# Kernel tuning notes

Hardware: AMD Instinct MI355X
Metric: run time of the kernel (lower is better)

Reference implementation:

```python
import jax, jax.numpy as jnp
import numpy as np

B, S, D, K = 128, 200, 128, 4
NQ, NC = 10000, 500


def setup_inputs() -> dict:
    key = jax.random.key(0)
    ks = jax.random.split(key, 20)
    f = jnp.float32
    inp = {}
    inp["question_seq"] = jax.random.randint(ks[0], (B, S), 0, NQ)
    inp["hint_attempt_seq"] = jax.random.randint(ks[1], (B, S), 0, 12)
    inp["correct_seq"] = jax.random.randint(ks[2], (B, S), 0, 2)
    inp["interval_time_seq"] = jax.random.randint(ks[3], (B, S), 0, 100)
    inp["use_time_seq"] = jax.random.randint(ks[4], (B, S), 0, 100)
    inp["q2c_table"] = jax.random.randint(ks[5], (NQ, K), 0, NC)
    inp["q2c_mask_table"] = jax.random.randint(ks[6], (NQ, K), 0, 2)
    s = 0.1
    inp["embed_question"] = jax.random.normal(ks[7], (NQ, D), f) * s
    inp["embed_question_disc"] = jax.random.normal(ks[8], (NQ, 1), f) * s
    inp["embed_concept"] = jax.random.normal(ks[9], (NC, D), f) * s
    inp["embed_interval_time"] = jax.random.normal(ks[10], (100, D), f) * s
    inp["embed_use_time"] = jax.random.normal(ks[11], (100, D), f) * s
    inp["embed_hint_attempt"] = jax.random.normal(ks[12], (12, D), f) * s
    inp["W_fuse"] = jax.random.normal(ks[13], (2 * D, D), f) / np.float32(np.sqrt(2 * D))
    inp["b_fuse"] = jnp.zeros((D,), f)
    inp["W_absorb"] = jax.random.normal(ks[14], (3 * D, D), f) / np.float32(np.sqrt(3 * D))
    inp["b_absorb"] = jnp.zeros((D,), f)
    inp["W_forget"] = jax.random.normal(ks[15], (3 * D, D), f) / np.float32(np.sqrt(3 * D))
    inp["b_forget"] = jnp.zeros((D,), f)
    inp["latent0"] = jax.random.normal(ks[16], (B, D), f) * 0.1  # xavier-init latent_pre
    return inp


def _cos(a, b, eps=1e-8):
    # torch.cosine_similarity semantics with eps clamp on each norm
    num = jnp.sum(a * b, axis=-1)
    na = jnp.sqrt(jnp.sum(a * a, axis=-1))
    nb = jnp.sqrt(jnp.sum(b * b, axis=-1))
    return num / (jnp.maximum(na, eps) * jnp.maximum(nb, eps))


def _forward(question_seq, hint_attempt_seq, correct_seq, interval_time_seq, use_time_seq,
             q2c_table, q2c_mask_table,
             embed_question, embed_question_disc, embed_concept, embed_interval_time,
             embed_use_time, embed_hint_attempt,
             W_fuse, b_fuse, W_absorb, b_absorb, W_forget, b_forget, latent0):
    f = latent0.dtype
    qe = embed_question[question_seq]                                # [B,S,D]
    qd = jax.nn.sigmoid(embed_question_disc[question_seq]) * 10.0    # [B,S,1]
    ce = jnp.broadcast_to(correct_seq.astype(f)[:, :, None], qe.shape)  # [B,S,D]
    ite = embed_interval_time[interval_time_seq]                     # [B,S,D]
    ute = embed_use_time[use_time_seq]                               # [B,S,D]
    hae = embed_hint_attempt[hint_attempt_seq]                       # [B,S,D]
    cp = embed_concept[q2c_table[question_seq]]                      # [B,S,K,D]
    m = q2c_mask_table[question_seq].astype(f)                       # [B,S,K]

    tm = lambda x: jnp.swapaxes(x, 0, 1)  # time-major for scan
    xs = (tm(qe[:, :-1]), tm(ce[:, :-1]), tm(ute[:, :-1]), tm(hae[:, :-1]), tm(ite[:, :-1]),
          tm(cp[:, :-1]), tm(cp[:, 1:]), tm(qd[:, 1:]), tm(m[:, :-1]))

    def step(lp, x):
        qe_t, ce_t, ute_t, hae_t, ite_t, cp_t, cp_t1, qd_t1, m_t = x
        inter = jnp.concatenate([qe_t, ce_t], axis=-1) @ W_fuse + b_fuse
        absorb = jnp.concatenate([inter, ute_t, hae_t], axis=-1) @ W_absorb + b_absorb
        forget = jax.nn.sigmoid(jnp.concatenate([lp, ite_t, inter], axis=-1) @ W_forget + b_forget)
        lc = lp * forget + absorb  # dropout p=0 -> identity
        qdiff = (_cos(qe_t[:, None, :], cp_t) + 1.0) * 0.5   # [B,K]
        uab = (_cos(lc[:, None, :], cp_t1) + 1.0) * 0.5      # [B,K]
        logit = qd_t1[:, 0] * jnp.sum((uab - qdiff) * m_t, axis=-1)  # [B]
        return lc, jax.nn.sigmoid(logit)

    _, ys = jax.lax.scan(step, latent0, xs)  # ys: [S-1, B]
    y = jnp.concatenate([ys.T, jnp.zeros((latent0.shape[0], 1), f)], axis=1)  # [B,S], last col 0
    return y


def reference(question_seq, hint_attempt_seq, correct_seq, interval_time_seq, use_time_seq,
              q2c_table, q2c_mask_table,
              embed_question, embed_question_disc, embed_concept, embed_interval_time,
              embed_use_time, embed_hint_attempt,
              W_fuse, b_fuse, W_absorb, b_absorb, W_forget, b_forget, latent0):
    return _forward(question_seq, hint_attempt_seq, correct_seq, interval_time_seq, use_time_seq,
                    q2c_table, q2c_mask_table,
                    embed_question, embed_question_disc, embed_concept, embed_interval_time,
                    embed_use_time, embed_hint_attempt,
                    W_fuse, b_fuse, W_absorb, b_absorb, W_forget, b_forget, latent0)
```

## Files before the change

### kernel.cpp

```cpp
#include <hip/hip_runtime.h>
#include <hip/hip_bf16.h>

typedef unsigned short u16;

#define Bb  128
#define Ss  200
#define Tt  199
#define Dd  128
#define Kk  4
#define NQq 10000
#define NCc 500
#define CHK 16
#define NCH 13

__device__ inline float bf2f(u16 u) {
    union { unsigned int i; float f; } x;
    x.i = ((unsigned int)u) << 16;
    return x.f;
}

__device__ inline float ldf(const void* p, int i, int m) {
    if (m) return ((const float*)p)[i];
    return bf2f(((const u16*)p)[i]);
}

__device__ inline void stf(void* p, int i, int m, float v) {
    if (m) ((float*)p)[i] = v;
    else ((__hip_bfloat16*)p)[i] = __float2bfloat16(v);
}

__device__ inline int clampi(int v, int lo, int hi) {
    return v < lo ? lo : (v > hi ? hi : v);
}

__device__ inline float wave_red(float v) {
#pragma unroll
    for (int m = 32; m >= 1; m >>= 1) v += __shfl_xor(v, m);
    return v;
}

__device__ inline float4 f4add(float4 a, float4 b) {
    return make_float4(a.x + b.x, a.y + b.y, a.z + b.z, a.w + b.w);
}
__device__ inline float4 f4fma(float s, float4 a, float4 b) {
    return make_float4(fmaf(s, a.x, b.x), fmaf(s, a.y, b.y),
                       fmaf(s, a.z, b.z), fmaf(s, a.w, b.w));
}

__device__ inline int detect_mode(const void* Eq) {
    const u16* q = (const u16*)Eq;
    const int l = threadIdx.x & 63;
    float mx = 0.f;
#pragma unroll
    for (int k = 0; k < 4; ++k) {
        float a = fabsf(bf2f(q[l * 4 + k]));
        if (!(a == a)) a = 3.0e38f;
        mx = fmaxf(mx, a);
    }
#pragma unroll
    for (int s = 32; s >= 1; s >>= 1) mx = fmaxf(mx, __shfl_xor(mx, s));
    return (mx > 1.0e6f) ? 1 : 0;
}

__global__ __launch_bounds__(128) void k_prep(
    const void* Eq, const void* Wf, const void* Wa, const void* Wg,
    const void* bfu, const void* ba, const void* bg,
    const void* Eut, const void* Eha, const void* Eit, const void* Ec,
    float* cnorm, float* BabT, float* BfgT,
    float* vA0, float* vA1, float* vF0, float* vF1,
    float* PA_ut, float* PA_ha, float* PF_it) {
    const int m = detect_mode(Eq);
    const int bi = blockIdx.x, tid = threadIdx.x;
    __shared__ float cs2s[128];
    __shared__ float tmp[2];
    if (bi < 500) {
        const int c = bi;
        float v = ldf(Ec, c * 128 + tid, m);
        float s = wave_red(v * v);
        if ((tid & 63) == 0) tmp[tid >> 6] = s;
        __syncthreads();
        if (tid == 0) cnorm[c] = fmaxf(sqrtf(tmp[0] + tmp[1]), 1e-8f);
    } else if (bi < 628) {
        const int r = bi - 500;
        float acc = 0.f;
        for (int j = 0; j < 128; ++j)
            acc += ldf(Wf, r * 128 + j, m) * ldf(Wa, j * 128 + tid, m);
        BabT[r * 128 + tid] = acc;
    } else if (bi < 756) {
        const int r = bi - 628;
        float acc = 0.f;
        for (int j = 0; j < 128; ++j)
            acc += ldf(Wf, r * 128 + j, m) * ldf(Wg, (256 + j) * 128 + tid, m);
        BfgT[r * 128 + tid] = acc;
    } else if (bi == 756) {
        float s = 0.f;
        for (int r = 0; r < 128; ++r) s += ldf(Wf, (128 + r) * 128 + tid, m);
        cs2s[tid] = s;
        __syncthreads();
        float a0 = 0.f, a1 = 0.f;
        for (int j = 0; j < 128; ++j) {
            float wv = ldf(Wa, j * 128 + tid, m);
            a0 += ldf(bfu, j, m) * wv;
            a1 += cs2s[j] * wv;
        }
        vA0[tid] = a0 + ldf(ba, tid, m);
        vA1[tid] = a1;
    } else if (bi == 757) {
        float s = 0.f;
        for (int r = 0; r < 128; ++r) s += ldf(Wf, (128 + r) * 128 + tid, m);
        cs2s[tid] = s;
        __syncthreads();
        float a0 = 0.f, a1 = 0.f;
        for (int j = 0; j < 128; ++j) {
            float wv = ldf(Wg, (256 + j) * 128 + tid, m);
            a0 += ldf(bfu, j, m) * wv;
            a1 += cs2s[j] * wv;
        }
        vF0[tid] = a0 + ldf(bg, tid, m);
        vF1[tid] = a1;
    } else if (bi < 858) {
        const int r = bi - 758;
        float acc = 0.f;
        for (int j = 0; j < 128; ++j)
            acc += ldf(Eut, r * 128 + j, m) * ldf(Wa, (128 + j) * 128 + tid, m);
        PA_ut[r * 128 + tid] = acc;
    } else if (bi < 870) {
        const int r = bi - 858;
        float acc = 0.f;
        for (int j = 0; j < 128; ++j)
            acc += ldf(Eha, r * 128 + j, m) * ldf(Wa, (256 + j) * 128 + tid, m);
        PA_ha[r * 128 + tid] = acc;
    } else {
        const int r = bi - 870;
        float acc = 0.f;
        for (int j = 0; j < 128; ++j)
            acc += ldf(Eit, r * 128 + j, m) * ldf(Wg, (128 + j) * 128 + tid, m);
        PF_it[r * 128 + tid] = acc;
    }
}

__global__ __launch_bounds__(256) void k_mid(
    const void* Eq, const void* Eqd, const void* Ec,
    const int* q2c, const int* q2cm,
    const float* BabT, const float* BfgT, const float* cnorm,
    float* PA_q, float* PF_q, float* qdm, float* qd10) {
    const int m = detect_mode(Eq);
    const int tid = threadIdx.x;
    const int bi = blockIdx.x;
    if (bi < 313) {
        __shared__ float At[32][36];
        __shared__ float Bt0[32][128];
        __shared__ float Bt1[32][128];
        const int r0 = bi * 32;
        float acc0[2][8], acc1[2][8];
#pragma unroll
        for (int j = 0; j < 2; ++j)
#pragma unroll
            for (int i = 0; i < 8; ++i) { acc0[j][i] = 0.f; acc1[j][i] = 0.f; }
        const int tx = tid & 15, ty = tid >> 4;
        for (int ks = 0; ks < 4; ++ks) {
            {
                const int row = tid >> 3, seg = tid & 7;
                const int q = clampi(r0 + row, 0, NQq - 1);
                const int ei = q * 128 + ks * 32 + seg * 4;
                float* dst = &At[row][seg * 4];
                if (m) {
                    float4 v = *(const float4*)((const float*)Eq + ei);
                    dst[0] = v.x; dst[1] = v.y; dst[2] = v.z; dst[3] = v.w;
                } else {
                    uint2 v = *(const uint2*)((const u16*)Eq + ei);
                    dst[0] = bf2f((u16)(v.x & 0xffff)); dst[1] = bf2f((u16)(v.x >> 16));
                    dst[2] = bf2f((u16)(v.y & 0xffff)); dst[3] = bf2f((u16)(v.y >> 16));
                }
            }
            {
                const float4* s0 = (const float4*)(BabT + ks * 32 * 128);
                const float4* s1 = (const float4*)(BfgT + ks * 32 * 128);
                float4* d0 = (float4*)&Bt0[0][0];
                float4* d1 = (float4*)&Bt1[0][0];
#pragma unroll
                for (int k = 0; k < 4; ++k) {
                    d0[tid + k * 256] = s0[tid + k * 256];
                    d1[tid + k * 256] = s1[tid + k * 256];
                }
            }
            __syncthreads();
#pragma unroll
            for (int kk = 0; kk < 32; kk += 4) {
                float a_[2][4];
                *(float4*)&a_[0][0] = *(const float4*)&At[ty * 2 + 0][kk];
                *(float4*)&a_[1][0] = *(const float4*)&At[ty * 2 + 1][kk];
#pragma unroll
                for (int q = 0; q < 4; ++q) {
                    float4 b0 = *(const float4*)&Bt0[kk + q][tx * 8];
                    float4 b1 = *(const float4*)&Bt0[kk + q][tx * 8 + 4];
                    float4 c0 = *(const float4*)&Bt1[kk + q][tx * 8];
                    float4 c1 = *(const float4*)&Bt1[kk + q][tx * 8 + 4];
#pragma unroll
                    for (int j = 0; j < 2; ++j) {
                        const float av = a_[j][q];
                        acc0[j][0] += av * b0.x; acc0[j][1] += av * b0.y;
                        acc0[j][2] += av * b0.z; acc0[j][3] += av * b0.w;
                        acc0[j][4] += av * b1.x; acc0[j][5] += av * b1.y;
                        acc0[j][6] += av * b1.z; acc0[j][7] += av * b1.w;
                        acc1[j][0] += av * c0.x; acc1[j][1] += av * c0.y;
                        acc1[j][2] += av * c0.z; acc1[j][3] += av * c0.w;
                        acc1[j][4] += av * c1.x; acc1[j][5] += av * c1.y;
                        acc1[j][6] += av * c1.z; acc1[j][7] += av * c1.w;
                    }
                }
            }
            __syncthreads();
        }
#pragma unroll
        for (int j = 0; j < 2; ++j) {
            const int q = r0 + ty * 2 + j;
            if (q < NQq) {
                float* oa = PA_q + q * 128 + tx * 8;
                float* of = PF_q + q * 128 + tx * 8;
#pragma unroll
                for (int i = 0; i < 8; ++i) { oa[i] = acc0[j][i]; of[i] = acc1[j][i]; }
            }
        }
    } else {
        const int wv = tid >> 6, lane = tid & 63;
        const int q = (bi - 313) * 4 + wv;
        const float qa = ldf(Eq, q * 128 + lane, m);
        const float qb = ldf(Eq, q * 128 + 64 + lane, m);
        const float nqc = fmaxf(sqrtf(wave_red(qa * qa + qb * qb)), 1e-8f);
        const int4 cc = ((const int4*)q2c)[q];
        const int4 mm = ((const int4*)q2cm)[q];
        const int cks[4] = {clampi(cc.x, 0, NCc - 1), clampi(cc.y, 0, NCc - 1),
                            clampi(cc.z, 0, NCc - 1), clampi(cc.w, 0, NCc - 1)};
        const int ms[4]  = {mm.x, mm.y, mm.z, mm.w};
        float qs = 0.f;
#pragma unroll
        for (int k = 0; k < 4; ++k) {
            const int ck = cks[k];
            float dot = wave_red(qa * ldf(Ec, ck * 128 + lane, m) +
                                 qb * ldf(Ec, ck * 128 + 64 + lane, m));
            qs += (float)ms[k] * (0.5f * dot / (nqc * cnorm[ck]) + 0.5f);
        }
        if (lane == 0) {
            qdm[q] = qs;
            qd10[q] = 10.f / (1.f + __expf(-ldf(Eqd, q, m)));
        }
    }
}

__global__ __launch_bounds__(256) void p4_scan(
    const int* q_seq, const int* ut_seq, const int* ha_seq, const int* it_seq,
    const int* c_seq,
    const void* Eq, const void* Wg, const void* L0,
    const float* PA_q, const float* PA_ut, const float* PA_ha,
    const float* PF_q, const float* PF_it,
    const float* vA0, const float* vA1, const float* vF0, const float* vF1,
    float* lc_seq) {
    const int m = detect_mode(Eq);
    const int b = blockIdx.x;
    const int tid = threadIdx.x;
    const int wv = tid >> 6, l = tid & 63;
    const int d0 = 2 * l;
    const int ib = wv << 5;
    const int dd = ib + (l & 31);

    __shared__ float part[2][4][128];
    __shared__ float st_ab[CHK * 128];
    __shared__ float st_pf[CHK * 128];

    float wA[32], wB[32];
#pragma unroll
    for (int k = 0; k < 32; ++k) {
        wA[k] = ldf(Wg, (ib + k) * 128 + d0, m);
        wB[k] = ldf(Wg, (ib + k) * 128 + d0 + 1, m);
    }
    float lc = (l < 32) ? ldf(L0, b * 128 + dd, m) : 0.f;

    const int srow = tid >> 4, seg = tid & 15;
    const int off8 = seg * 8;
    const float4 A0a = *(const float4*)(vA0 + off8), A0b = *(const float4*)(vA0 + off8 + 4);
    const float4 A1a = *(const float4*)(vA1 + off8), A1b = *(const float4*)(vA1 + off8 + 4);
    const float4 F0a = *(const float4*)(vF0 + off8), F0b = *(const float4*)(vF0 + off8 + 4);
    const float4 F1a = *(const float4*)(vF1 + off8), F1b = *(const float4*)(vF1 + off8 + 4);

    float4 qa0, qa1, ua0, ua1, ga0, ga1, qf0, qf1, if0, if1;
    float cf;
#define LOAD_CHUNK(C)                                                          \
    {                                                                          \
        int tt = (C) * CHK + srow; if (tt > Tt - 1) tt = Tt - 1;               \
        const int base = b * Ss + tt;                                          \
        const int qt = clampi(q_seq[base], 0, NQq - 1);                        \
        const int ut = clampi(ut_seq[base], 0, 99);                            \
        const int ha = clampi(ha_seq[base], 0, 11);                            \
        const int it = clampi(it_seq[base], 0, 99);                            \
        cf = (float)c_seq[base];                                               \
        const float* pq = PA_q + qt * 128 + off8;                              \
        qa0 = *(const float4*)pq; qa1 = *(const float4*)(pq + 4);              \
        const float* pu = PA_ut + ut * 128 + off8;                             \
        ua0 = *(const float4*)pu; ua1 = *(const float4*)(pu + 4);              \
        const float* ph = PA_ha + ha * 128 + off8;                             \
        ga0 = *(const float4*)ph; ga1 = *(const float4*)(ph + 4);              \
        const float* pf = PF_q + qt * 128 + off8;                              \
        qf0 = *(const float4*)pf; qf1 = *(const float4*)(pf + 4);              \
        const float* pi = PF_it + it * 128 + off8;                             \
        if0 = *(const float4*)pi; if1 = *(const float4*)(pi + 4);              \
    }

    LOAD_CHUNK(0)
    float lcbuf[CHK];
    int par = 0;

    for (int c = 0; c < NCH; ++c) {
        __syncthreads();
        {
            float4 ab0 = f4fma(cf, A1a, f4add(f4add(qa0, ua0), f4add(ga0, A0a)));
            float4 ab1 = f4fma(cf, A1b, f4add(f4add(qa1, ua1), f4add(ga1, A0b)));
            float4 pf0 = f4fma(cf, F1a, f4add(qf0, f4add(if0, F0a)));
            float4 pf1 = f4fma(cf, F1b, f4add(qf1, f4add(if1, F0b)));
            float4* sa = (float4*)(st_ab + srow * 128 + off8);
            sa[0] = ab0; sa[1] = ab1;
            float4* sp = (float4*)(st_pf + srow * 128 + off8);
            sp[0] = pf0; sp[1] = pf1;
        }
        if (c + 1 < NCH) LOAD_CHUNK(c + 1)
        __syncthreads();

#pragma unroll
        for (int s = 0; s < CHK; ++s) {
            float pa = 0.f, pb = 0.f;
#pragma unroll
            for (int k = 0; k < 32; ++k) {
                const float u = __uint_as_float(
                    __builtin_amdgcn_readlane(__float_as_uint(lc), k));
                pa = fmaf(u, wA[k], pa);
                pb = fmaf(u, wB[k], pb);
            }
            *(float2*)&part[par][wv][d0] = make_float2(pa, pb);
            __syncthreads();
            if (l < 32) {
                const float fs = part[par][0][dd] + part[par][1][dd]
                               + part[par][2][dd] + part[par][3][dd];
                const float ab = st_ab[(s << 7) + dd];
                const float pf = st_pf[(s << 7) + dd];
                const float fg = 1.f / (1.f + __expf(-(fs + pf)));
                lc = lc * fg + ab;
                lcbuf[s] = lc;
            }
            par ^= 1;
        }
        if (l < 32) {
#pragma unroll
            for (int s = 0; s < CHK; ++s) {
                const int t = c * CHK + s;
                if (t < Tt)
                    lc_seq[((long)t * 128 + b) * 128 + dd] = lcbuf[s];
            }
        }
    }
#undef LOAD_CHUNK
}

__global__ __launch_bounds__(256) void p5_out(
    const int* q_seq, const int* q2c, const int* q2cm,
    const float* lc_seq, const float* qdm, const float* qd10,
    const float* cnorm, const void* Eq, const void* Ec, void* out) {
    const int m = detect_mode(Eq);
    const int wv = threadIdx.x >> 6, lane = threadIdx.x & 63;
    const int r = blockIdx.x * 4 + wv;
    const int t = r >> 7, b = r & 127;
    const int qt  = clampi(q_seq[b * Ss + t], 0, NQq - 1);
    const int qt1 = clampi(q_seq[b * Ss + t + 1], 0, NQq - 1);
    const int4 mm = ((const int4*)q2cm)[qt];
    int4 ci = ((const int4*)q2c)[qt1];
    const int c0 = clampi(ci.x, 0, NCc - 1), c1 = clampi(ci.y, 0, NCc - 1);
    const int c2 = clampi(ci.z, 0, NCc - 1), c3 = clampi(ci.w, 0, NCc - 1);
    const float la = lc_seq[(long)r * 128 + lane];
    const float lb = lc_seq[(long)r * 128 + 64 + lane];
    float nl = la * la + lb * lb;
    float d0 = la * ldf(Ec, c0 * 128 + lane, m) + lb * ldf(Ec, c0 * 128 + 64 + lane, m);
    float d1 = la * ldf(Ec, c1 * 128 + lane, m) + lb * ldf(Ec, c1 * 128 + 64 + lane, m);
    float d2 = la * ldf(Ec, c2 * 128 + lane, m) + lb * ldf(Ec, c2 * 128 + 64 + lane, m);
    float d3 = la * ldf(Ec, c3 * 128 + lane, m) + lb * ldf(Ec, c3 * 128 + 64 + lane, m);
#pragma unroll
    for (int s = 32; s >= 1; s >>= 1) {
        nl += __shfl_xor(nl, s);
        d0 += __shfl_xor(d0, s); d1 += __shfl_xor(d1, s);
        d2 += __shfl_xor(d2, s); d3 += __shfl_xor(d3, s);
    }
    if (lane == 0) {
        const float inl = 1.f / fmaxf(sqrtf(nl), 1e-8f);
        const float accv = (float)mm.x * (0.5f * d0 * inl / cnorm[c0] + 0.5f)
                         + (float)mm.y * (0.5f * d1 * inl / cnorm[c1] + 0.5f)
                         + (float)mm.z * (0.5f * d2 * inl / cnorm[c2] + 0.5f)
                         + (float)mm.w * (0.5f * d3 * inl / cnorm[c3] + 0.5f);
        const float logit = qd10[qt1] * (accv - qdm[qt]);
        stf(out, b * Ss + t, m, 1.f / (1.f + __expf(-logit)));
        if (t == 0) stf(out, b * Ss + 199, m, 0.f);
    }
}

extern "C" void kernel_launch(void* const* d_in, const int* in_sizes, int n_in,
                              void* d_out, int out_size, void* d_ws, size_t ws_size,
                              hipStream_t stream) {
    (void)in_sizes; (void)n_in; (void)out_size; (void)ws_size;
    const int* q_seq  = (const int*)d_in[0];
    const int* ha_seq = (const int*)d_in[1];
    const int* c_seq  = (const int*)d_in[2];
    const int* it_seq = (const int*)d_in[3];
    const int* ut_seq = (const int*)d_in[4];
    const int* q2c    = (const int*)d_in[5];
    const int* q2cm   = (const int*)d_in[6];
    const void* Eq   = d_in[7];
    const void* Eqd  = d_in[8];
    const void* Ec   = d_in[9];
    const void* Eit  = d_in[10];
    const void* Eut  = d_in[11];
    const void* Eha  = d_in[12];
    const void* Wf   = d_in[13];
    const void* bfu  = d_in[14];
    const void* Wa   = d_in[15];
    const void* ba   = d_in[16];
    const void* Wg   = d_in[17];
    const void* bg   = d_in[18];
    const void* L0   = d_in[19];

    float* cnorm = (float*)d_ws;
    float* vA0   = cnorm + 512;
    float* vA1   = vA0 + 128;
    float* vF0   = vA1 + 128;
    float* vF1   = vF0 + 128;
    float* BabT  = vF1 + 128;
    float* BfgT  = BabT + 16384;
    float* PA_ut = BfgT + 16384;
    float* PA_ha = PA_ut + 12800;
    float* PF_it = PA_ha + 1536;
    float* qdm   = PF_it + 12800;
    float* qd10  = qdm + 10016;
    float* PA_q  = qd10 + 10016;
    float* PF_q  = PA_q + 1280000;
    float* lc_seq= PF_q + 1280000;

    hipLaunchKernelGGL(k_prep, dim3(970), dim3(128), 0, stream,
                       Eq, Wf, Wa, Wg, bfu, ba, bg, Eut, Eha, Eit, Ec,
                       cnorm, BabT, BfgT, vA0, vA1, vF0, vF1, PA_ut, PA_ha, PF_it);
    hipLaunchKernelGGL(k_mid, dim3(2813), dim3(256), 0, stream,
                       Eq, Eqd, Ec, q2c, q2cm, BabT, BfgT, cnorm,
                       PA_q, PF_q, qdm, qd10);
    hipLaunchKernelGGL(p4_scan, dim3(Bb), dim3(256), 0, stream,
                       q_seq, ut_seq, ha_seq, it_seq, c_seq, Eq, Wg, L0,
                       PA_q, PA_ut, PA_ha, PF_q, PF_it,
                       vA0, vA1, vF0, vF1, lc_seq);
    hipLaunchKernelGGL(p5_out, dim3(Tt * Bb / 4), dim3(256), 0, stream,
                       q_seq, q2c, q2cm, lc_seq, qdm, qd10, cnorm, Eq, Ec, d_out);
}
```

Measured before the change: 235.4 us.

## Fuse all four stages into one persistent cooperative kernel with grid syncs

Replaces the four separate launches (prep, mid, scan, output) with one cooperative kernel of 512 blocks that loops over job indices and separates the phases with grid-wide syncs. Concept norms are now recomputed inline instead of stored in a cnorm table, and the prep jobs pair two outputs per 256-thread block. This targets launch overhead and idle gaps between small dependent kernels. In exchange, work is throttled to the persistent grid size, and the serial scan phase runs on only 128 blocks while the rest wait at the final barrier.

```diff
diff --git a/kernel.cpp b/kernel.cpp
--- a/kernel.cpp
+++ b/kernel.cpp
@@ -1,17 +1,19 @@
 #include <hip/hip_runtime.h>
 #include <hip/hip_bf16.h>
+#include <hip/hip_cooperative_groups.h>
+
+namespace cg = cooperative_groups;
 
 typedef unsigned short u16;
 
 #define Bb  128
 #define Ss  200
 #define Tt  199
-#define Dd  128
-#define Kk  4
 #define NQq 10000
 #define NCc 500
 #define CHK 16
 #define NCH 13
+#define GRID 512
 
 __device__ inline float bf2f(u16 u) {
     union { unsigned int i; float f; } x;
@@ -62,340 +64,339 @@
     return (mx > 1.0e6f) ? 1 : 0;
 }
 
-__global__ __launch_bounds__(128) void k_prep(
-    const void* Eq, const void* Wf, const void* Wa, const void* Wg,
-    const void* bfu, const void* ba, const void* bg,
-    const void* Eut, const void* Eha, const void* Eit, const void* Ec,
-    float* cnorm, float* BabT, float* BfgT,
-    float* vA0, float* vA1, float* vF0, float* vF1,
-    float* PA_ut, float* PA_ha, float* PF_it) {
-    const int m = detect_mode(Eq);
-    const int bi = blockIdx.x, tid = threadIdx.x;
-    __shared__ float cs2s[128];
-    __shared__ float tmp[2];
-    if (bi < 500) {
-        const int c = bi;
-        float v = ldf(Ec, c * 128 + tid, m);
-        float s = wave_red(v * v);
-        if ((tid & 63) == 0) tmp[tid >> 6] = s;
-        __syncthreads();
-        if (tid == 0) cnorm[c] = fmaxf(sqrtf(tmp[0] + tmp[1]), 1e-8f);
-    } else if (bi < 628) {
-        const int r = bi - 500;
-        float acc = 0.f;
-        for (int j = 0; j < 128; ++j)
-            acc += ldf(Wf, r * 128 + j, m) * ldf(Wa, j * 128 + tid, m);
-        BabT[r * 128 + tid] = acc;
-    } else if (bi < 756) {
-        const int r = bi - 628;
-        float acc = 0.f;
-        for (int j = 0; j < 128; ++j)
-            acc += ldf(Wf, r * 128 + j, m) * ldf(Wg, (256 + j) * 128 + tid, m);
-        BfgT[r * 128 + tid] = acc;
-    } else if (bi == 756) {
-        float s = 0.f;
-        for (int r = 0; r < 128; ++r) s += ldf(Wf, (128 + r) * 128 + tid, m);
-        cs2s[tid] = s;
-        __syncthreads();
-        float a0 = 0.f, a1 = 0.f;
-        for (int j = 0; j < 128; ++j) {
-            float wv = ldf(Wa, j * 128 + tid, m);
-            a0 += ldf(bfu, j, m) * wv;
-            a1 += cs2s[j] * wv;
-        }
-        vA0[tid] = a0 + ldf(ba, tid, m);
-        vA1[tid] = a1;
-    } else if (bi == 757) {
-        float s = 0.f;
-        for (int r = 0; r < 128; ++r) s += ldf(Wf, (128 + r) * 128 + tid, m);
-        cs2s[tid] = s;
-        __syncthreads();
-        float a0 = 0.f, a1 = 0.f;
-        for (int j = 0; j < 128; ++j) {
-            float wv = ldf(Wg, (256 + j) * 128 + tid, m);
-            a0 += ldf(bfu, j, m) * wv;
-            a1 += cs2s[j] * wv;
-        }
-        vF0[tid] = a0 + ldf(bg, tid, m);
-        vF1[tid] = a1;
-    } else if (bi < 858) {
-        const int r = bi - 758;
-        float acc = 0.f;
-        for (int j = 0; j < 128; ++j)
-            acc += ldf(Eut, r * 128 + j, m) * ldf(Wa, (128 + j) * 128 + tid, m);
-        PA_ut[r * 128 + tid] = acc;
-    } else if (bi < 870) {
-        const int r = bi - 858;
-        float acc = 0.f;
-        for (int j = 0; j < 128; ++j)
-            acc += ldf(Eha, r * 128 + j, m) * ldf(Wa, (256 + j) * 128 + tid, m);
-        PA_ha[r * 128 + tid] = acc;
-    } else {
-        const int r = bi - 870;
-        float acc = 0.f;
-        for (int j = 0; j < 128; ++j)
-            acc += ldf(Eit, r * 128 + j, m) * ldf(Wg, (128 + j) * 128 + tid, m);
-        PF_it[r * 128 + tid] = acc;
+struct KArgs {
+    const int *q_seq, *ha_seq, *c_seq, *it_seq, *ut_seq, *q2c, *q2cm;
+    const void *Eq, *Eqd, *Ec, *Eit, *Eut, *Eha;
+    const void *Wf, *bfu, *Wa, *ba, *Wg, *bg, *L0;
+    float *BabT, *BfgT, *vA0, *vA1, *vF0, *vF1;
+    float *PA_ut, *PA_ha, *PF_it, *qdm, *qd10, *PA_q, *PF_q, *lc_seq;
+    void* out;
+};
+
+__global__ __launch_bounds__(256, 4) void k_fused(KArgs a) {
+    cg::grid_group grid = cg::this_grid();
+    __shared__ __align__(16) float smemf[9344];
+    const int m = detect_mode(a.Eq);
+    const int tid = threadIdx.x;
+    const int nb = gridDim.x;
+
+    for (int job = blockIdx.x; job < 241; job += nb) {
+        if (job < 128) {
+            const int r = job, col = tid & 127;
+            float acc = 0.f;
+            if (tid < 128) {
+                for (int j = 0; j < 128; ++j)
+                    acc += ldf(a.Wf, r * 128 + j, m) * ldf(a.Wa, j * 128 + col, m);
+                a.BabT[r * 128 + col] = acc;
+            } else {
+                for (int j = 0; j < 128; ++j)
+                    acc += ldf(a.Wf, r * 128 + j, m) * ldf(a.Wg, (256 + j) * 128 + col, m);
+                a.BfgT[r * 128 + col] = acc;
+            }
+        } else if (job == 128) {
+            const int col = tid & 127;
+            if (tid < 128) {
+                float s = 0.f;
+                for (int r2 = 0; r2 < 128; ++r2) s += ldf(a.Wf, (128 + r2) * 128 + col, m);
+                smemf[col] = s;
+            }
+            __syncthreads();
+            float a0 = 0.f, a1 = 0.f;
+            if (tid < 128) {
+                for (int j = 0; j < 128; ++j) {
+                    const float wv = ldf(a.Wa, j * 128 + col, m);
+                    a0 += ldf(a.bfu, j, m) * wv;
+                    a1 += smemf[j] * wv;
+                }
+                a.vA0[col] = a0 + ldf(a.ba, col, m);
+                a.vA1[col] = a1;
+            } else {
+                for (int j = 0; j < 128; ++j) {
+                    const float wv = ldf(a.Wg, (256 + j) * 128 + col, m);
+                    a0 += ldf(a.bfu, j, m) * wv;
+                    a1 += smemf[j] * wv;
+                }
+                a.vF0[col] = a0 + ldf(a.bg, col, m);
+                a.vF1[col] = a1;
+            }
+            __syncthreads();
+        } else if (job < 229) {
+            const int r = job - 129, col = tid & 127;
+            float acc = 0.f;
+            if (tid < 128) {
+                for (int j = 0; j < 128; ++j)
+                    acc += ldf(a.Eut, r * 128 + j, m) * ldf(a.Wa, (128 + j) * 128 + col, m);
+                a.PA_ut[r * 128 + col] = acc;
+            } else {
+                for (int j = 0; j < 128; ++j)
+                    acc += ldf(a.Eit, r * 128 + j, m) * ldf(a.Wg, (128 + j) * 128 + col, m);
+                a.PF_it[r * 128 + col] = acc;
+            }
+        } else {
+            const int r = job - 229;
+            if (tid < 128) {
+                float acc = 0.f;
+                for (int j = 0; j < 128; ++j)
+                    acc += ldf(a.Eha, r * 128 + j, m) * ldf(a.Wa, (256 + j) * 128 + tid, m);
+                a.PA_ha[r * 128 + tid] = acc;
+            }
+        }
     }
-}
-
-__global__ __launch_bounds__(256) void k_mid(
-    const void* Eq, const void* Eqd, const void* Ec,
-    const int* q2c, const int* q2cm,
-    const float* BabT, const float* BfgT, const float* cnorm,
-    float* PA_q, float* PF_q, float* qdm, float* qd10) {
-    const int m = detect_mode(Eq);
-    const int tid = threadIdx.x;
-    const int bi = blockIdx.x;
-    if (bi < 313) {
-        __shared__ float At[32][36];
-        __shared__ float Bt0[32][128];
-        __shared__ float Bt1[32][128];
-        const int r0 = bi * 32;
-        float acc0[2][8], acc1[2][8];
-#pragma unroll
-        for (int j = 0; j < 2; ++j)
-#pragma unroll
-            for (int i = 0; i < 8; ++i) { acc0[j][i] = 0.f; acc1[j][i] = 0.f; }
-        const int tx = tid & 15, ty = tid >> 4;
-        for (int ks = 0; ks < 4; ++ks) {
+    __threadfence();
+    grid.sync();
+
+    {
+        float* At  = smemf;
+        float* Bt0 = smemf + 1152;
+        float* Bt1 = smemf + 5248;
+        for (int job = blockIdx.x; job < 2813; job += nb) {
+            if (job < 313) {
+                const int r0 = job * 32;
+                float acc0[2][8], acc1[2][8];
+#pragma unroll
+                for (int j = 0; j < 2; ++j)
+#pragma unroll
+                    for (int i = 0; i < 8; ++i) { acc0[j][i] = 0.f; acc1[j][i] = 0.f; }
+                const int tx = tid & 15, ty = tid >> 4;
+                for (int ks = 0; ks < 4; ++ks) {
+                    {
+                        const int row = tid >> 3, seg = tid & 7;
+                        const int q = clampi(r0 + row, 0, NQq - 1);
+                        const int ei = q * 128 + ks * 32 + seg * 4;
+                        float* dst = At + row * 36 + seg * 4;
+                        if (m) {
+                            float4 v = *(const float4*)((const float*)a.Eq + ei);
+                            dst[0] = v.x; dst[1] = v.y; dst[2] = v.z; dst[3] = v.w;
+                        } else {
+                            uint2 v = *(const uint2*)((const u16*)a.Eq + ei);
+                            dst[0] = bf2f((u16)(v.x & 0xffff)); dst[1] = bf2f((u16)(v.x >> 16));
+                            dst[2] = bf2f((u16)(v.y & 0xffff)); dst[3] = bf2f((u16)(v.y >> 16));
+                        }
+                    }
+                    {
+                        const float4* s0 = (const float4*)(a.BabT + ks * 32 * 128);
+                        const float4* s1 = (const float4*)(a.BfgT + ks * 32 * 128);
+                        float4* d0 = (float4*)Bt0;
+                        float4* d1 = (float4*)Bt1;
+#pragma unroll
+                        for (int k = 0; k < 4; ++k) {
+                            d0[tid + k * 256] = s0[tid + k * 256];
+                            d1[tid + k * 256] = s1[tid + k * 256];
+                        }
+                    }
+                    __syncthreads();
+#pragma unroll
+                    for (int kk = 0; kk < 32; kk += 4) {
+                        float a_[2][4];
+                        *(float4*)&a_[0][0] = *(const float4*)(At + (ty * 2 + 0) * 36 + kk);
+                        *(float4*)&a_[1][0] = *(const float4*)(At + (ty * 2 + 1) * 36 + kk);
+#pragma unroll
+                        for (int q = 0; q < 4; ++q) {
+                            float4 b0 = *(const float4*)(Bt0 + (kk + q) * 128 + tx * 8);
+                            float4 b1 = *(const float4*)(Bt0 + (kk + q) * 128 + tx * 8 + 4);
+                            float4 c0 = *(const float4*)(Bt1 + (kk + q) * 128 + tx * 8);
+                            float4 c1 = *(const float4*)(Bt1 + (kk + q) * 128 + tx * 8 + 4);
+#pragma unroll
+                            for (int j = 0; j < 2; ++j) {
+                                const float av = a_[j][q];
+                                acc0[j][0] += av * b0.x; acc0[j][1] += av * b0.y;
+                                acc0[j][2] += av * b0.z; acc0[j][3] += av * b0.w;
+                                acc0[j][4] += av * b1.x; acc0[j][5] += av * b1.y;
+                                acc0[j][6] += av * b1.z; acc0[j][7] += av * b1.w;
+                                acc1[j][0] += av * c0.x; acc1[j][1] += av * c0.y;
+                                acc1[j][2] += av * c0.z; acc1[j][3] += av * c0.w;
+                                acc1[j][4] += av * c1.x; acc1[j][5] += av * c1.y;
+                                acc1[j][6] += av * c1.z; acc1[j][7] += av * c1.w;
+                            }
+                        }
+                    }
+                    __syncthreads();
+                }
+#pragma unroll
+                for (int j = 0; j < 2; ++j) {
+                    const int q = r0 + ty * 2 + j;
+                    if (q < NQq) {
+                        float* oa = a.PA_q + q * 128 + tx * 8;
+                        float* of = a.PF_q + q * 128 + tx * 8;
+#pragma unroll
+                        for (int i = 0; i < 8; ++i) { oa[i] = acc0[j][i]; of[i] = acc1[j][i]; }
+                    }
+                }
+            } else {
+                const int wv = tid >> 6, lane = tid & 63;
+                const int q = (job - 313) * 4 + wv;
+                const float qa = ldf(a.Eq, q * 128 + lane, m);
+                const float qb = ldf(a.Eq, q * 128 + 64 + lane, m);
+                const float nqc = fmaxf(sqrtf(wave_red(qa * qa + qb * qb)), 1e-8f);
+                const int4 cc = ((const int4*)a.q2c)[q];
+                const int4 mm = ((const int4*)a.q2cm)[q];
+                const int cks[4] = {clampi(cc.x, 0, NCc - 1), clampi(cc.y, 0, NCc - 1),
+                                    clampi(cc.z, 0, NCc - 1), clampi(cc.w, 0, NCc - 1)};
+                const int ms[4]  = {mm.x, mm.y, mm.z, mm.w};
+                float qs = 0.f;
+#pragma unroll
+                for (int k = 0; k < 4; ++k) {
+                    const int ck = cks[k];
+                    const float ea = ldf(a.Ec, ck * 128 + lane, m);
+                    const float eb = ldf(a.Ec, ck * 128 + 64 + lane, m);
+                    const float dot = wave_red(qa * ea + qb * eb);
+                    const float nn = fmaxf(sqrtf(wave_red(ea * ea + eb * eb)), 1e-8f);
+                    qs += (float)ms[k] * (0.5f * dot / (nqc * nn) + 0.5f);
+                }
+                if (lane == 0) {
+                    a.qdm[q] = qs;
+                    a.qd10[q] = 10.f / (1.f + __expf(-ldf(a.Eqd, q, m)));
+                }
+            }
+        }
+    }
+    __threadfence();
+    grid.sync();
+
+    if (blockIdx.x < 128) {
+        float* part  = smemf;
+        float* st_ab = smemf + 1024;
+        float* st_pf = smemf + 3072;
+        const int b = blockIdx.x;
+        const int wv = tid >> 6, l = tid & 63;
+        const int d0 = 2 * l;
+        const int ib = wv << 5;
+        const int dd = ib + (l & 31);
+
+        float wA[32], wB[32];
+#pragma unroll
+        for (int k = 0; k < 32; ++k) {
+            wA[k] = ldf(a.Wg, (ib + k) * 128 + d0, m);
+            wB[k] = ldf(a.Wg, (ib + k) * 128 + d0 + 1, m);
+        }
+        float lc = (l < 32) ? ldf(a.L0, b * 128 + dd, m) : 0.f;
+
+        const int srow = tid >> 4, seg = tid & 15;
+        const int off8 = seg * 8;
+        const float4 A0a = *(const float4*)(a.vA0 + off8), A0b = *(const float4*)(a.vA0 + off8 + 4);
+        const float4 A1a = *(const float4*)(a.vA1 + off8), A1b = *(const float4*)(a.vA1 + off8 + 4);
+        const float4 F0a = *(const float4*)(a.vF0 + off8), F0b = *(const float4*)(a.vF0 + off8 + 4);
+        const float4 F1a = *(const float4*)(a.vF1 + off8), F1b = *(const float4*)(a.vF1 + off8 + 4);
+
+        float4 qa0, qa1, ua0, ua1, ga0, ga1, qf0, qf1, if0, if1;
+        float cf;
+#define LOAD_CHUNK(C)                                                          \
+        {                                                                      \
+            int tt = (C) * CHK + srow; if (tt > Tt - 1) tt = Tt - 1;           \
+            const int base = b * Ss + tt;                                      \
+            const int qt = clampi(a.q_seq[base], 0, NQq - 1);                  \
+            const int ut = clampi(a.ut_seq[base], 0, 99);                      \
+            const int ha = clampi(a.ha_seq[base], 0, 11);                      \
+            const int it = clampi(a.it_seq[base], 0, 99);                      \
+            cf = (float)a.c_seq[base];                                         \
+            const float* pq = a.PA_q + qt * 128 + off8;                        \
+            qa0 = *(const float4*)pq; qa1 = *(const float4*)(pq + 4);          \
+            const float* pu = a.PA_ut + ut * 128 + off8;                       \
+            ua0 = *(const float4*)pu; ua1 = *(const float4*)(pu + 4);          \
+            const float* ph = a.PA_ha + ha * 128 + off8;                       \
+            ga0 = *(const float4*)ph; ga1 = *(const float4*)(ph + 4);          \
+            const float* pf = a.PF_q + qt * 128 + off8;                        \
+            qf0 = *(const float4*)pf; qf1 = *(const float4*)(pf + 4);          \
+            const float* pi = a.PF_it + it * 128 + off8;                       \
+            if0 = *(const float4*)pi; if1 = *(const float4*)(pi + 4);          \
+        }
+
+        LOAD_CHUNK(0)
+        float lcbuf[CHK];
+        int par = 0;
+
+        for (int c = 0; c < NCH; ++c) {
+            __syncthreads();
             {
-                const int row = tid >> 3, seg = tid & 7;
-                const int q = clampi(r0 + row, 0, NQq - 1);
-                const int ei = q * 128 + ks * 32 + seg * 4;
-                float* dst = &At[row][seg * 4];
-                if (m) {
-                    float4 v = *(const float4*)((const float*)Eq + ei);
-                    dst[0] = v.x; dst[1] = v.y; dst[2] = v.z; dst[3] = v.w;
-                } else {
-                    uint2 v = *(const uint2*)((const u16*)Eq + ei);
-                    dst[0] = bf2f((u16)(v.x & 0xffff)); dst[1] = bf2f((u16)(v.x >> 16));
-                    dst[2] = bf2f((u16)(v.y & 0xffff)); dst[3] = bf2f((u16)(v.y >> 16));
-                }
-            }
-            {
-                const float4* s0 = (const float4*)(BabT + ks * 32 * 128);
-                const float4* s1 = (const float4*)(BfgT + ks * 32 * 128);
-                float4* d0 = (float4*)&Bt0[0][0];
-                float4* d1 = (float4*)&Bt1[0][0];
-#pragma unroll
-                for (int k = 0; k < 4; ++k) {
-                    d0[tid + k * 256] = s0[tid + k * 256];
-                    d1[tid + k * 256] = s1[tid + k * 256];
-                }
-            }
+                float4 ab0 = f4fma(cf, A1a, f4add(f4add(qa0, ua0), f4add(ga0, A0a)));
+                float4 ab1 = f4fma(cf, A1b, f4add(f4add(qa1, ua1), f4add(ga1, A0b)));
+                float4 pf0 = f4fma(cf, F1a, f4add(qf0, f4add(if0, F0a)));
+                float4 pf1 = f4fma(cf, F1b, f4add(qf1, f4add(if1, F0b)));
+                float4* sa = (float4*)(st_ab + srow * 128 + off8);
+                sa[0] = ab0; sa[1] = ab1;
+                float4* sp = (float4*)(st_pf + srow * 128 + off8);
+                sp[0] = pf0; sp[1] = pf1;
+            }
+            if (c + 1 < NCH) LOAD_CHUNK(c + 1)
             __syncthreads();
-#pragma unroll
-            for (int kk = 0; kk < 32; kk += 4) {
-                float a_[2][4];
-                *(float4*)&a_[0][0] = *(const float4*)&At[ty * 2 + 0][kk];
-                *(float4*)&a_[1][0] = *(const float4*)&At[ty * 2 + 1][kk];
-#pragma unroll
-                for (int q = 0; q < 4; ++q) {
-                    float4 b0 = *(const float4*)&Bt0[kk + q][tx * 8];
-                    float4 b1 = *(const float4*)&Bt0[kk + q][tx * 8 + 4];
-                    float4 c0 = *(const float4*)&Bt1[kk + q][tx * 8];
-                    float4 c1 = *(const float4*)&Bt1[kk + q][tx * 8 + 4];
-#pragma unroll
-                    for (int j = 0; j < 2; ++j) {
-                        const float av = a_[j][q];
-                        acc0[j][0] += av * b0.x; acc0[j][1] += av * b0.y;
-                        acc0[j][2] += av * b0.z; acc0[j][3] += av * b0.w;
-                        acc0[j][4] += av * b1.x; acc0[j][5] += av * b1.y;
-                        acc0[j][6] += av * b1.z; acc0[j][7] += av * b1.w;
-                        acc1[j][0] += av * c0.x; acc1[j][1] += av * c0.y;
-                        acc1[j][2] += av * c0.z; acc1[j][3] += av * c0.w;
-                        acc1[j][4] += av * c1.x; acc1[j][5] += av * c1.y;
-                        acc1[j][6] += av * c1.z; acc1[j][7] += av * c1.w;
-                    }
-                }
-            }
-            __syncthreads();
-        }
-#pragma unroll
-        for (int j = 0; j < 2; ++j) {
-            const int q = r0 + ty * 2 + j;
-            if (q < NQq) {
-                float* oa = PA_q + q * 128 + tx * 8;
-                float* of = PF_q + q * 128 + tx * 8;
-#pragma unroll
-                for (int i = 0; i < 8; ++i) { oa[i] = acc0[j][i]; of[i] = acc1[j][i]; }
-            }
-        }
-    } else {
+
+#pragma unroll
+            for (int s = 0; s < CHK; ++s) {
+                float pa = 0.f, pb = 0.f;
+#pragma unroll
+                for (int k = 0; k < 32; ++k) {
+                    const float u = __uint_as_float(
+                        __builtin_amdgcn_readlane(__float_as_uint(lc), k));
+                    pa = fmaf(u, wA[k], pa);
+                    pb = fmaf(u, wB[k], pb);
+                }
+                *(float2*)(part + par * 512 + wv * 128 + d0) = make_float2(pa, pb);
+                __syncthreads();
+                if (l < 32) {
+                    const float fs = part[par * 512 + 0 * 128 + dd] + part[par * 512 + 1 * 128 + dd]
+                                   + part[par * 512 + 2 * 128 + dd] + part[par * 512 + 3 * 128 + dd];
+                    const float ab = st_ab[(s << 7) + dd];
+                    const float pf = st_pf[(s << 7) + dd];
+                    const float fg = 1.f / (1.f + __expf(-(fs + pf)));
+                    lc = lc * fg + ab;
+                    lcbuf[s] = lc;
+                }
+                par ^= 1;
+            }
+            if (l < 32) {
+#pragma unroll
+                for (int s = 0; s < CHK; ++s) {
+                    const int t = c * CHK + s;
+                    if (t < Tt)
+                        a.lc_seq[((long)t * 128 + b) * 128 + dd] = lcbuf[s];
+                }
+            }
+        }
+#undef LOAD_CHUNK
+    }
+    __threadfence();
+    grid.sync();
+
+    for (int job = blockIdx.x; job < 6368; job += nb) {
         const int wv = tid >> 6, lane = tid & 63;
-        const int q = (bi - 313) * 4 + wv;
-        const float qa = ldf(Eq, q * 128 + lane, m);
-        const float qb = ldf(Eq, q * 128 + 64 + lane, m);
-        const float nqc = fmaxf(sqrtf(wave_red(qa * qa + qb * qb)), 1e-8f);
-        const int4 cc = ((const int4*)q2c)[q];
-        const int4 mm = ((const int4*)q2cm)[q];
-        const int cks[4] = {clampi(cc.x, 0, NCc - 1), clampi(cc.y, 0, NCc - 1),
-                            clampi(cc.z, 0, NCc - 1), clampi(cc.w, 0, NCc - 1)};
-        const int ms[4]  = {mm.x, mm.y, mm.z, mm.w};
-        float qs = 0.f;
-#pragma unroll
-        for (int k = 0; k < 4; ++k) {
-            const int ck = cks[k];
-            float dot = wave_red(qa * ldf(Ec, ck * 128 + lane, m) +
-                                 qb * ldf(Ec, ck * 128 + 64 + lane, m));
-            qs += (float)ms[k] * (0.5f * dot / (nqc * cnorm[ck]) + 0.5f);
+        const int r = job * 4 + wv;
+        const int t = r >> 7, b = r & 127;
+        const int qt  = clampi(a.q_seq[b * Ss + t], 0, NQq - 1);
+        const int qt1 = clampi(a.q_seq[b * Ss + t + 1], 0, NQq - 1);
+        const int4 mm = ((const int4*)a.q2cm)[qt];
+        int4 ci = ((const int4*)a.q2c)[qt1];
+        const int c0 = clampi(ci.x, 0, NCc - 1), c1 = clampi(ci.y, 0, NCc - 1);
+        const int c2 = clampi(ci.z, 0, NCc - 1), c3 = clampi(ci.w, 0, NCc - 1);
+        const float la = a.lc_seq[(long)r * 128 + lane];
+        const float lb = a.lc_seq[(long)r * 128 + 64 + lane];
+        const float e0a = ldf(a.Ec, c0 * 128 + lane, m), e0b = ldf(a.Ec, c0 * 128 + 64 + lane, m);
+        const float e1a = ldf(a.Ec, c1 * 128 + lane, m), e1b = ldf(a.Ec, c1 * 128 + 64 + lane, m);
+        const float e2a = ldf(a.Ec, c2 * 128 + lane, m), e2b = ldf(a.Ec, c2 * 128 + 64 + lane, m);
+        const float e3a = ldf(a.Ec, c3 * 128 + lane, m), e3b = ldf(a.Ec, c3 * 128 + 64 + lane, m);
+        float nl = la * la + lb * lb;
+        float d0 = la * e0a + lb * e0b, n0 = e0a * e0a + e0b * e0b;
+        float d1 = la * e1a + lb * e1b, n1 = e1a * e1a + e1b * e1b;
+        float d2 = la * e2a + lb * e2b, n2 = e2a * e2a + e2b * e2b;
+        float d3 = la * e3a + lb * e3b, n3 = e3a * e3a + e3b * e3b;
+#pragma unroll
+        for (int s = 32; s >= 1; s >>= 1) {
+            nl += __shfl_xor(nl, s);
+            d0 += __shfl_xor(d0, s); d1 += __shfl_xor(d1, s);
+            d2 += __shfl_xor(d2, s); d3 += __shfl_xor(d3, s);
+            n0 += __shfl_xor(n0, s); n1 += __shfl_xor(n1, s);
+            n2 += __shfl_xor(n2, s); n3 += __shfl_xor(n3, s);
         }
         if (lane == 0) {
-            qdm[q] = qs;
-            qd10[q] = 10.f / (1.f + __expf(-ldf(Eqd, q, m)));
-        }
-    }
-}
-
-__global__ __launch_bounds__(256) void p4_scan(
-    const int* q_seq, const int* ut_seq, const int* ha_seq, const int* it_seq,
-    const int* c_seq,
-    const void* Eq, const void* Wg, const void* L0,
-    const float* PA_q, const float* PA_ut, const float* PA_ha,
-    const float* PF_q, const float* PF_it,
-    const float* vA0, const float* vA1, const float* vF0, const float* vF1,
-    float* lc_seq) {
-    const int m = detect_mode(Eq);
-    const int b = blockIdx.x;
-    const int tid = threadIdx.x;
-    const int wv = tid >> 6, l = tid & 63;
-    const int d0 = 2 * l;
-    const int ib = wv << 5;
-    const int dd = ib + (l & 31);
-
-    __shared__ float part[2][4][128];
-    __shared__ float st_ab[CHK * 128];
-    __shared__ float st_pf[CHK * 128];
-
-    float wA[32], wB[32];
-#pragma unroll
-    for (int k = 0; k < 32; ++k) {
-        wA[k] = ldf(Wg, (ib + k) * 128 + d0, m);
-        wB[k] = ldf(Wg, (ib + k) * 128 + d0 + 1, m);
-    }
-    float lc = (l < 32) ? ldf(L0, b * 128 + dd, m) : 0.f;
-
-    const int srow = tid >> 4, seg = tid & 15;
-    const int off8 = seg * 8;
-    const float4 A0a = *(const float4*)(vA0 + off8), A0b = *(const float4*)(vA0 + off8 + 4);
-    const float4 A1a = *(const float4*)(vA1 + off8), A1b = *(const float4*)(vA1 + off8 + 4);
-    const float4 F0a = *(const float4*)(vF0 + off8), F0b = *(const float4*)(vF0 + off8 + 4);
-    const float4 F1a = *(const float4*)(vF1 + off8), F1b = *(const float4*)(vF1 + off8 + 4);
-
-    float4 qa0, qa1, ua0, ua1, ga0, ga1, qf0, qf1, if0, if1;
-    float cf;
-#define LOAD_CHUNK(C)                                                          \
-    {                                                                          \
-        int tt = (C) * CHK + srow; if (tt > Tt - 1) tt = Tt - 1;               \
-        const int base = b * Ss + tt;                                          \
-        const int qt = clampi(q_seq[base], 0, NQq - 1);                        \
-        const int ut = clampi(ut_seq[base], 0, 99);                            \
-        const int ha = clampi(ha_seq[base], 0, 11);                            \
-        const int it = clampi(it_seq[base], 0, 99);                            \
-        cf = (float)c_seq[base];                                               \
-        const float* pq = PA_q + qt * 128 + off8;                              \
-        qa0 = *(const float4*)pq; qa1 = *(const float4*)(pq + 4);              \
-        const float* pu = PA_ut + ut * 128 + off8;                             \
-        ua0 = *(const float4*)pu; ua1 = *(const float4*)(pu + 4);              \
-        const float* ph = PA_ha + ha * 128 + off8;                             \
-        ga0 = *(const float4*)ph; ga1 = *(const float4*)(ph + 4);              \
-        const float* pf = PF_q + qt * 128 + off8;                              \
-        qf0 = *(const float4*)pf; qf1 = *(const float4*)(pf + 4);              \
-        const float* pi = PF_it + it * 128 + off8;                             \
-        if0 = *(const float4*)pi; if1 = *(const float4*)(pi + 4);              \
-    }
-
-    LOAD_CHUNK(0)
-    float lcbuf[CHK];
-    int par = 0;
-
-    for (int c = 0; c < NCH; ++c) {
-        __syncthreads();
-        {
-            float4 ab0 = f4fma(cf, A1a, f4add(f4add(qa0, ua0), f4add(ga0, A0a)));
-            float4 ab1 = f4fma(cf, A1b, f4add(f4add(qa1, ua1), f4add(ga1, A0b)));
-            float4 pf0 = f4fma(cf, F1a, f4add(qf0, f4add(if0, F0a)));
-            float4 pf1 = f4fma(cf, F1b, f4add(qf1, f4add(if1, F0b)));
-            float4* sa = (float4*)(st_ab + srow * 128 + off8);
-            sa[0] = ab0; sa[1] = ab1;
-            float4* sp = (float4*)(st_pf + srow * 128 + off8);
-            sp[0] = pf0; sp[1] = pf1;
-        }
-        if (c + 1 < NCH) LOAD_CHUNK(c + 1)
-        __syncthreads();
-
-#pragma unroll
-        for (int s = 0; s < CHK; ++s) {
-            float pa = 0.f, pb = 0.f;
-#pragma unroll
-            for (int k = 0; k < 32; ++k) {
-                const float u = __uint_as_float(
-                    __builtin_amdgcn_readlane(__float_as_uint(lc), k));
-                pa = fmaf(u, wA[k], pa);
-                pb = fmaf(u, wB[k], pb);
-            }
-            *(float2*)&part[par][wv][d0] = make_float2(pa, pb);
-            __syncthreads();
-            if (l < 32) {
-                const float fs = part[par][0][dd] + part[par][1][dd]
-                               + part[par][2][dd] + part[par][3][dd];
-                const float ab = st_ab[(s << 7) + dd];
-                const float pf = st_pf[(s << 7) + dd];
-                const float fg = 1.f / (1.f + __expf(-(fs + pf)));
-                lc = lc * fg + ab;
-                lcbuf[s] = lc;
-            }
-            par ^= 1;
-        }
-        if (l < 32) {
-#pragma unroll
-            for (int s = 0; s < CHK; ++s) {
-                const int t = c * CHK + s;
-                if (t < Tt)
-                    lc_seq[((long)t * 128 + b) * 128 + dd] = lcbuf[s];
-            }
-        }
-    }
-#undef LOAD_CHUNK
-}
-
-__global__ __launch_bounds__(256) void p5_out(
-    const int* q_seq, const int* q2c, const int* q2cm,
-    const float* lc_seq, const float* qdm, const float* qd10,
-    const float* cnorm, const void* Eq, const void* Ec, void* out) {
-    const int m = detect_mode(Eq);
-    const int wv = threadIdx.x >> 6, lane = threadIdx.x & 63;
-    const int r = blockIdx.x * 4 + wv;
-    const int t = r >> 7, b = r & 127;
-    const int qt  = clampi(q_seq[b * Ss + t], 0, NQq - 1);
-    const int qt1 = clampi(q_seq[b * Ss + t + 1], 0, NQq - 1);
-    const int4 mm = ((const int4*)q2cm)[qt];
-    int4 ci = ((const int4*)q2c)[qt1];
-    const int c0 = clampi(ci.x, 0, NCc - 1), c1 = clampi(ci.y, 0, NCc - 1);
-    const int c2 = clampi(ci.z, 0, NCc - 1), c3 = clampi(ci.w, 0, NCc - 1);
-    const float la = lc_seq[(long)r * 128 + lane];
-    const float lb = lc_seq[(long)r * 128 + 64 + lane];
-    float nl = la * la + lb * lb;
-    float d0 = la * ldf(Ec, c0 * 128 + lane, m) + lb * ldf(Ec, c0 * 128 + 64 + lane, m);
-    float d1 = la * ldf(Ec, c1 * 128 + lane, m) + lb * ldf(Ec, c1 * 128 + 64 + lane, m);
-    float d2 = la * ldf(Ec, c2 * 128 + lane, m) + lb * ldf(Ec, c2 * 128 + 64 + lane, m);
-    float d3 = la * ldf(Ec, c3 * 128 + lane, m) + lb * ldf(Ec, c3 * 128 + 64 + lane, m);
-#pragma unroll
-    for (int s = 32; s >= 1; s >>= 1) {
-        nl += __shfl_xor(nl, s);
-        d0 += __shfl_xor(d0, s); d1 += __shfl_xor(d1, s);
-        d2 += __shfl_xor(d2, s); d3 += __shfl_xor(d3, s);
-    }
-    if (lane == 0) {
-        const float inl = 1.f / fmaxf(sqrtf(nl), 1e-8f);
-        const float accv = (float)mm.x * (0.5f * d0 * inl / cnorm[c0] + 0.5f)
-                         + (float)mm.y * (0.5f * d1 * inl / cnorm[c1] + 0.5f)
-                         + (float)mm.z * (0.5f * d2 * inl / cnorm[c2] + 0.5f)
-                         + (float)mm.w * (0.5f * d3 * inl / cnorm[c3] + 0.5f);
-        const float logit = qd10[qt1] * (accv - qdm[qt]);
-        stf(out, b * Ss + t, m, 1.f / (1.f + __expf(-logit)));
-        if (t == 0) stf(out, b * Ss + 199, m, 0.f);
+            const float inl = 1.f / fmaxf(sqrtf(nl), 1e-8f);
+            const float accv =
+                  (float)mm.x * (0.5f * d0 * inl / fmaxf(sqrtf(n0), 1e-8f) + 0.5f)
+                + (float)mm.y * (0.5f * d1 * inl / fmaxf(sqrtf(n1), 1e-8f) + 0.5f)
+                + (float)mm.z * (0.5f * d2 * inl / fmaxf(sqrtf(n2), 1e-8f) + 0.5f)
+                + (float)mm.w * (0.5f * d3 * inl / fmaxf(sqrtf(n3), 1e-8f) + 0.5f);
+            const float logit = a.qd10[qt1] * (accv - a.qdm[qt]);
+            stf(a.out, b * Ss + t, m, 1.f / (1.f + __expf(-logit)));
+            if (t == 0) stf(a.out, b * Ss + 199, m, 0.f);
+        }
     }
 }
 
@@ -403,53 +404,46 @@
                               void* d_out, int out_size, void* d_ws, size_t ws_size,
                               hipStream_t stream) {
     (void)in_sizes; (void)n_in; (void)out_size; (void)ws_size;
-    const int* q_seq  = (const int*)d_in[0];
-    const int* ha_seq = (const int*)d_in[1];
-    const int* c_seq  = (const int*)d_in[2];
-    const int* it_seq = (const int*)d_in[3];
-    const int* ut_seq = (const int*)d_in[4];
-    const int* q2c    = (const int*)d_in[5];
-    const int* q2cm   = (const int*)d_in[6];
-    const void* Eq   = d_in[7];
-    const void* Eqd  = d_in[8];
-    const void* Ec   = d_in[9];
-    const void* Eit  = d_in[10];
-    const void* Eut  = d_in[11];
-    const void* Eha  = d_in[12];
-    const void* Wf   = d_in[13];
-    const void* bfu  = d_in[14];
-    const void* Wa   = d_in[15];
-    const void* ba   = d_in[16];
-    const void* Wg   = d_in[17];
-    const void* bg   = d_in[18];
-    const void* L0   = d_in[19];
-
-    float* cnorm = (float*)d_ws;
-    float* vA0   = cnorm + 512;
-    float* vA1   = vA0 + 128;
-    float* vF0   = vA1 + 128;
-    float* vF1   = vF0 + 128;
-    float* BabT  = vF1 + 128;
-    float* BfgT  = BabT + 16384;
-    float* PA_ut = BfgT + 16384;
-    float* PA_ha = PA_ut + 12800;
-    float* PF_it = PA_ha + 1536;
-    float* qdm   = PF_it + 12800;
-    float* qd10  = qdm + 10016;
-    float* PA_q  = qd10 + 10016;
-    float* PF_q  = PA_q + 1280000;
-    float* lc_seq= PF_q + 1280000;
-
-    hipLaunchKernelGGL(k_prep, dim3(970), dim3(128), 0, stream,
-                       Eq, Wf, Wa, Wg, bfu, ba, bg, Eut, Eha, Eit, Ec,
-                       cnorm, BabT, BfgT, vA0, vA1, vF0, vF1, PA_ut, PA_ha, PF_it);
-    hipLaunchKernelGGL(k_mid, dim3(2813), dim3(256), 0, stream,
-                       Eq, Eqd, Ec, q2c, q2cm, BabT, BfgT, cnorm,
-                       PA_q, PF_q, qdm, qd10);
-    hipLaunchKernelGGL(p4_scan, dim3(Bb), dim3(256), 0, stream,
-                       q_seq, ut_seq, ha_seq, it_seq, c_seq, Eq, Wg, L0,
-                       PA_q, PA_ut, PA_ha, PF_q, PF_it,
-                       vA0, vA1, vF0, vF1, lc_seq);
-    hipLaunchKernelGGL(p5_out, dim3(Tt * Bb / 4), dim3(256), 0, stream,
-                       q_seq, q2c, q2cm, lc_seq, qdm, qd10, cnorm, Eq, Ec, d_out);
-}
+    KArgs a;
+    a.q_seq  = (const int*)d_in[0];
+    a.ha_seq = (const int*)d_in[1];
+    a.c_seq  = (const int*)d_in[2];
+    a.it_seq = (const int*)d_in[3];
+    a.ut_seq = (const int*)d_in[4];
+    a.q2c    = (const int*)d_in[5];
+    a.q2cm   = (const int*)d_in[6];
+    a.Eq  = d_in[7];
+    a.Eqd = d_in[8];
+    a.Ec  = d_in[9];
+    a.Eit = d_in[10];
+    a.Eut = d_in[11];
+    a.Eha = d_in[12];
+    a.Wf  = d_in[13];
+    a.bfu = d_in[14];
+    a.Wa  = d_in[15];
+    a.ba  = d_in[16];
+    a.Wg  = d_in[17];
+    a.bg  = d_in[18];
+    a.L0  = d_in[19];
+
+    float* ws   = (float*)d_ws;
+    a.vA0   = ws;
+    a.vA1   = a.vA0 + 128;
+    a.vF0   = a.vA1 + 128;
+    a.vF1   = a.vF0 + 128;
+    a.BabT  = a.vF1 + 128;
+    a.BfgT  = a.BabT + 16384;
+    a.PA_ut = a.BfgT + 16384;
+    a.PA_ha = a.PA_ut + 12800;
+    a.PF_it = a.PA_ha + 1536;
+    a.qdm   = a.PF_it + 12800;
+    a.qd10  = a.qdm + 10016;
+    a.PA_q  = a.qd10 + 10016;
+    a.PF_q  = a.PA_q + 1280000;
+    a.lc_seq= a.PF_q + 1280000;
+    a.out   = d_out;
+
+    void* params[] = { (void*)&a };
+    hipLaunchCooperativeKernel((const void*)k_fused, dim3(GRID), dim3(256),
+                               params, 0, stream);
+}
```

After: 685.1 us. +191.0%, slower.
